# Kernel optimization log

Measured on AMD Instinct MI355X. Metric: run time of the kernel, lower is better.

## Reference

```python
import jax, jax.numpy as jnp
import numpy as np

N_EMBED = 384
T_MAX = 256
EPS = 1e-5


def layer_norm(x, gamma, beta):
    mu = jnp.mean(x, axis=-1, keepdims=True)
    var = jnp.mean(jnp.square(x - mu), axis=-1, keepdims=True)
    return (x - mu) * jax.lax.rsqrt(var + EPS) * gamma + beta


def setup_inputs() -> dict:
    key = jax.random.key(0)
    ks = jax.random.split(key, 12)
    B, T, C = 128, 256, N_EMBED
    s = lambda fan_in: 1.0 / np.sqrt(fan_in)
    return {
        "x": jax.random.normal(ks[0], (B, T, C), dtype=jnp.float32),
        "W_attn": jax.random.uniform(ks[1], (C, 3 * C), minval=-s(C), maxval=s(C), dtype=jnp.float32),
        "b_attn": jax.random.uniform(ks[2], (3 * C,), minval=-s(C), maxval=s(C), dtype=jnp.float32),
        "W_proj": jax.random.uniform(ks[3], (C, C), minval=-s(C), maxval=s(C), dtype=jnp.float32),
        "b_proj": jax.random.uniform(ks[4], (C,), minval=-s(C), maxval=s(C), dtype=jnp.float32),
        "ln1_g": jnp.ones((C,), jnp.float32),
        "ln1_b": jnp.zeros((C,), jnp.float32),
        "ln2_g": jnp.ones((C,), jnp.float32),
        "ln2_b": jnp.zeros((C,), jnp.float32),
        "W1": jax.random.uniform(ks[5], (C, 4 * C), minval=-s(C), maxval=s(C), dtype=jnp.float32),
        "b1": jax.random.uniform(ks[6], (4 * C,), minval=-s(C), maxval=s(C), dtype=jnp.float32),
        "W2": jax.random.uniform(ks[7], (4 * C, C), minval=-s(4 * C), maxval=s(4 * C), dtype=jnp.float32),
        "b2": jax.random.uniform(ks[8], (4 * C,)[:1] and (C,), minval=-s(4 * C), maxval=s(4 * C), dtype=jnp.float32),
    }


def reference(x, W_attn, b_attn, W_proj, b_proj, ln1_g, ln1_b, ln2_g, ln2_b, W1, b1, W2, b2):
    B, T, C = x.shape
    # --- pre-LN single-head causal self-attention ---
    h = layer_norm(x, ln1_g, ln1_b)
    qkv = h @ W_attn + b_attn                      # [B,T,3C]
    q, k, v = jnp.split(qkv, 3, axis=-1)           # each [B,T,C]
    att = jnp.einsum('btc,bsc->bts', q, k) * (1.0 / jnp.sqrt(jnp.float32(C)))
    causal = jnp.tril(jnp.ones((T, T), bool))
    att = jnp.where(causal, att, -jnp.inf)
    att = jax.nn.softmax(att, axis=-1)             # dropout is identity (eval)
    y = jnp.einsum('bts,bsc->btc', att, v)
    x = x + (y @ W_proj + b_proj)
    # --- pre-LN MLP ---
    h2 = layer_norm(x, ln2_g, ln2_b)
    x = x + (jax.nn.relu(h2 @ W1 + b1) @ W2 + b2)
    return x
```

## Files before the change

kernel.cpp:

```cpp
#include <hip/hip_runtime.h>
#include <hip/hip_bf16.h>

#define C_EMB 384
#define T_SEQ 256
#define B_BATCH 128
#define M_ROWS (B_BATCH * T_SEQ)
#define QKV_LD 1152
#define BK 64

typedef __bf16 bf16_8 __attribute__((ext_vector_type(8)));
typedef float f32x4 __attribute__((ext_vector_type(4)));

__device__ __forceinline__ void load16_lds(const __bf16* g, __bf16* l) {
    __builtin_amdgcn_global_load_lds(
        (const __attribute__((address_space(1))) unsigned int*)g,
        (__attribute__((address_space(3))) unsigned int*)l, 16, 0, 0);
}

__global__ __launch_bounds__(256) void cast_all_kernel(const float* __restrict__ Wa,
                                                       const float* __restrict__ Wp,
                                                       const float* __restrict__ W1,
                                                       const float* __restrict__ W2,
                                                       __bf16* __restrict__ Wa_t,
                                                       __bf16* __restrict__ Wp_t,
                                                       __bf16* __restrict__ W1_t,
                                                       __bf16* __restrict__ W2_t) {
    int bid = blockIdx.x;
    const float* W; __bf16* Wt; int K, N, tx_n;
    if (bid < 432)      { W = Wa; Wt = Wa_t; K = 384;  N = 1152; tx_n = 36; }
    else if (bid < 576) { bid -= 432; W = Wp; Wt = Wp_t; K = 384;  N = 384;  tx_n = 12; }
    else if (bid < 1152){ bid -= 576; W = W1; Wt = W1_t; K = 384;  N = 1536; tx_n = 48; }
    else                { bid -= 1152; W = W2; Wt = W2_t; K = 1536; N = 384;  tx_n = 12; }
    int n0 = (bid % tx_n) * 32, k0 = (bid / tx_n) * 32;

    __shared__ float t[32][33];
    int tx = threadIdx.x & 31, ty = threadIdx.x >> 5;
#pragma unroll
    for (int i = 0; i < 4; ++i)
        t[ty + i * 8][tx] = W[(size_t)(k0 + ty + i * 8) * N + n0 + tx];
    __syncthreads();
#pragma unroll
    for (int i = 0; i < 4; ++i) {
        int n = ty + i * 8;
        Wt[(size_t)(n0 + n) * K + k0 + tx] = (__bf16)t[tx][n];
    }
}

__global__ __launch_bounds__(384) void ln_kernel(const float* __restrict__ x,
                                                 const float* __restrict__ g,
                                                 const float* __restrict__ bta,
                                                 __bf16* __restrict__ out) {
    int row = blockIdx.x;
    int c = threadIdx.x;
    float v = x[(size_t)row * C_EMB + c];

    __shared__ float red[6];
    float s = v;
#pragma unroll
    for (int o = 32; o; o >>= 1) s += __shfl_down(s, o);
    if ((c & 63) == 0) red[c >> 6] = s;
    __syncthreads();
    float mu = (red[0] + red[1] + red[2] + red[3] + red[4] + red[5]) * (1.0f / C_EMB);

    float d = v - mu;
    float s2 = d * d;
#pragma unroll
    for (int o = 32; o; o >>= 1) s2 += __shfl_down(s2, o);
    __syncthreads();
    if ((c & 63) == 0) red[c >> 6] = s2;
    __syncthreads();
    float var = (red[0] + red[1] + red[2] + red[3] + red[4] + red[5]) * (1.0f / C_EMB);

    out[(size_t)row * C_EMB + c] = (__bf16)(d * rsqrtf(var + 1e-5f) * g[c] + bta[c]);
}

template <int K, int NFULL, bool RELU, bool ACCUM>
__global__ __launch_bounds__(512, 1) void gemm_pipe(const __bf16* __restrict__ A,
                                                    const __bf16* __restrict__ Bt,
                                                    const float* __restrict__ bias,
                                                    void* __restrict__ out_) {
    __shared__ __align__(16) __bf16 At[2][128 * 64];
    __shared__ __align__(16) __bf16 Bs[2][384 * 64];

    int tid = threadIdx.x;
    int wave = tid >> 6, lane = tid & 63;
    int wr = wave >> 1, wc = wave & 1;
    int quad = lane >> 4, l16 = lane & 15;
    int bm = blockIdx.y * 128;
    int n0 = blockIdx.x * 384;
    int srow = lane >> 3;
    int sunit = (lane & 7) ^ srow;

    const __bf16* asrc0 = A + (size_t)(bm + srow) * K + sunit * 8;
    const __bf16* bsrc0 = Bt + (size_t)(n0 + srow) * K + sunit * 8;

    auto stage = [&](int buf, int k0) {
#pragma unroll
        for (int t = 0; t < 2; ++t) {
            int g = t * 8 + wave;
            load16_lds(asrc0 + (size_t)(g * 8) * K + k0, &At[buf][g * 8 * 64]);
        }
#pragma unroll
        for (int t = 0; t < 6; ++t) {
            int g = t * 8 + wave;
            load16_lds(bsrc0 + (size_t)(g * 8) * K + k0, &Bs[buf][g * 8 * 64]);
        }
    };

    f32x4 acc[2][12] = {};

    stage(0, 0);
    asm volatile("s_waitcnt vmcnt(0)" ::: "memory");
    __builtin_amdgcn_sched_barrier(0);
    __builtin_amdgcn_s_barrier();

#pragma unroll 2
    for (int kt = 0; kt < K / BK; ++kt) {
        int cur = kt & 1;
        if (kt < K / BK - 1) stage(cur ^ 1, (kt + 1) * BK);

        bf16_8 af[2][2];
#pragma unroll
        for (int p = 0; p < 2; ++p)
#pragma unroll
            for (int i = 0; i < 2; ++i) {
                int row = wr * 32 + i * 16 + l16;
                int u = (p * 4 + quad) ^ (row & 7);
                af[i][p] = *reinterpret_cast<const bf16_8*>(&At[cur][row * 64 + u * 8]);
            }
#pragma unroll
        for (int p = 0; p < 2; ++p)
#pragma unroll
            for (int j = 0; j < 12; ++j) {
                int row = wc * 192 + j * 16 + l16;
                int u = (p * 4 + quad) ^ (row & 7);
                bf16_8 bf = *reinterpret_cast<const bf16_8*>(&Bs[cur][row * 64 + u * 8]);
                acc[0][j] = __builtin_amdgcn_mfma_f32_16x16x32_bf16(af[0][p], bf, acc[0][j], 0, 0, 0);
                acc[1][j] = __builtin_amdgcn_mfma_f32_16x16x32_bf16(af[1][p], bf, acc[1][j], 0, 0, 0);
            }

        asm volatile("s_waitcnt vmcnt(0)" ::: "memory");
        __builtin_amdgcn_sched_barrier(0);
        __builtin_amdgcn_s_barrier();
    }

#pragma unroll
    for (int i = 0; i < 2; ++i)
#pragma unroll
        for (int r = 0; r < 4; ++r) {
            int m = bm + wr * 32 + i * 16 + quad * 4 + r;
#pragma unroll
            for (int j = 0; j < 12; ++j) {
                int n = n0 + wc * 192 + j * 16 + l16;
                float v = acc[i][j][r] + bias[n];
                if (RELU) v = fmaxf(v, 0.0f);
                if (ACCUM) {
                    float* o = &((float*)out_)[(size_t)m * NFULL + n];
                    *o = *o + v;
                } else {
                    ((__bf16*)out_)[(size_t)m * NFULL + n] = (__bf16)v;
                }
            }
        }
}

template <int K, int NFULL, bool RELU, bool ACCUM>
__global__ __launch_bounds__(256, 2) void gemm_pipe2(const __bf16* __restrict__ A,
                                                     const __bf16* __restrict__ Bt,
                                                     const float* __restrict__ bias,
                                                     void* __restrict__ out_) {
    __shared__ __align__(16) __bf16 At[2][128 * 64];
    __shared__ __align__(16) __bf16 Bs[2][192 * 64];

    int tid = threadIdx.x;
    int wave = tid >> 6, lane = tid & 63;
    int quad = lane >> 4, l16 = lane & 15;
    int bm = blockIdx.y * 128;
    int n0 = blockIdx.x * 192;
    int srow = lane >> 3;
    int sunit = (lane & 7) ^ srow;

    const __bf16* asrc0 = A + (size_t)(bm + srow) * K + sunit * 8;
    const __bf16* bsrc0 = Bt + (size_t)(n0 + srow) * K + sunit * 8;

    auto stage = [&](int buf, int k0) {
#pragma unroll
        for (int t = 0; t < 4; ++t) {
            int g = t * 4 + wave;
            load16_lds(asrc0 + (size_t)(g * 8) * K + k0, &At[buf][g * 8 * 64]);
        }
#pragma unroll
        for (int t = 0; t < 6; ++t) {
            int g = t * 4 + wave;
            load16_lds(bsrc0 + (size_t)(g * 8) * K + k0, &Bs[buf][g * 8 * 64]);
        }
    };

    f32x4 acc[2][12] = {};

    stage(0, 0);
    asm volatile("s_waitcnt vmcnt(0)" ::: "memory");
    __builtin_amdgcn_sched_barrier(0);
    __builtin_amdgcn_s_barrier();

#pragma unroll 2
    for (int kt = 0; kt < K / BK; ++kt) {
        int cur = kt & 1;
        if (kt < K / BK - 1) stage(cur ^ 1, (kt + 1) * BK);

        bf16_8 af[2][2];
#pragma unroll
        for (int p = 0; p < 2; ++p)
#pragma unroll
            for (int i = 0; i < 2; ++i) {
                int row = wave * 32 + i * 16 + l16;
                int u = (p * 4 + quad) ^ (row & 7);
                af[i][p] = *reinterpret_cast<const bf16_8*>(&At[cur][row * 64 + u * 8]);
            }
#pragma unroll
        for (int p = 0; p < 2; ++p)
#pragma unroll
            for (int j = 0; j < 12; ++j) {
                int row = j * 16 + l16;
                int u = (p * 4 + quad) ^ (row & 7);
                bf16_8 bf = *reinterpret_cast<const bf16_8*>(&Bs[cur][row * 64 + u * 8]);
                acc[0][j] = __builtin_amdgcn_mfma_f32_16x16x32_bf16(af[0][p], bf, acc[0][j], 0, 0, 0);
                acc[1][j] = __builtin_amdgcn_mfma_f32_16x16x32_bf16(af[1][p], bf, acc[1][j], 0, 0, 0);
            }

        asm volatile("s_waitcnt vmcnt(0)" ::: "memory");
        __builtin_amdgcn_sched_barrier(0);
        __builtin_amdgcn_s_barrier();
    }

#pragma unroll
    for (int i = 0; i < 2; ++i)
#pragma unroll
        for (int r = 0; r < 4; ++r) {
            int m = bm + wave * 32 + i * 16 + quad * 4 + r;
#pragma unroll
            for (int j = 0; j < 12; ++j) {
                int n = n0 + j * 16 + l16;
                float v = acc[i][j][r] + bias[n];
                if (RELU) v = fmaxf(v, 0.0f);
                if (ACCUM) {
                    float* o = &((float*)out_)[(size_t)m * NFULL + n];
                    *o = *o + v;
                } else {
                    ((__bf16*)out_)[(size_t)m * NFULL + n] = (__bf16)v;
                }
            }
        }
}

__global__ __launch_bounds__(256) void proj_ln_kernel(const __bf16* __restrict__ A,
                                                      const __bf16* __restrict__ Bt,
                                                      const float* __restrict__ bias,
                                                      const float* __restrict__ resid,
                                                      const float* __restrict__ lng,
                                                      const float* __restrict__ lnb,
                                                      float* __restrict__ out,
                                                      __bf16* __restrict__ h) {
    __shared__ __align__(16) __bf16 As[2 * 64 * 32];
    __shared__ __align__(16) __bf16 Bs[2 * 384 * 32];
    __shared__ float red[2][2][64];

    int tid = threadIdx.x;
    int wave = tid >> 6, lane = tid & 63;
    int wr = wave >> 1, wc = wave & 1;
    int quad = lane >> 4, l16 = lane & 15;
    int bm = blockIdx.x * 64;
    int lrow = lane >> 2, lcol = (lane & 3) * 8;

    f32x4 acc[2][12] = {};

    for (int k0 = 0; k0 < C_EMB; k0 += BK) {
        const __bf16* Ab = A + (size_t)bm * C_EMB + k0;
        const __bf16* Bb = Bt + k0;
#pragma unroll
        for (int p = 0; p < 2; ++p) {
            {
                int r0 = wave * 16;
                load16_lds(Ab + (size_t)(r0 + lrow) * C_EMB + p * 32 + lcol,
                           &As[p * 64 * 32 + r0 * 32]);
            }
#pragma unroll
            for (int i = 0; i < 6; ++i) {
                int r0 = (i * 4 + wave) * 16;
                load16_lds(Bb + (size_t)(r0 + lrow) * C_EMB + p * 32 + lcol,
                           &Bs[p * 384 * 32 + r0 * 32]);
            }
        }
        __syncthreads();

        bf16_8 af[2][2], bf[12][2];
#pragma unroll
        for (int p = 0; p < 2; ++p) {
#pragma unroll
            for (int i = 0; i < 2; ++i)
                af[i][p] = *reinterpret_cast<const bf16_8*>(
                    &As[p * 64 * 32 + (wr * 32 + i * 16 + l16) * 32 + quad * 8]);
#pragma unroll
            for (int j = 0; j < 12; ++j)
                bf[j][p] = *reinterpret_cast<const bf16_8*>(
                    &Bs[p * 384 * 32 + (wc * 192 + j * 16 + l16) * 32 + quad * 8]);
        }
#pragma unroll
        for (int i = 0; i < 2; ++i)
#pragma unroll
            for (int j = 0; j < 12; ++j) {
                acc[i][j] = __builtin_amdgcn_mfma_f32_16x16x32_bf16(af[i][0], bf[j][0], acc[i][j], 0, 0, 0);
                acc[i][j] = __builtin_amdgcn_mfma_f32_16x16x32_bf16(af[i][1], bf[j][1], acc[i][j], 0, 0, 0);
            }
        __syncthreads();
    }

    float bia[12], gg[12], bb[12];
#pragma unroll
    for (int j = 0; j < 12; ++j) {
        int n = wc * 192 + j * 16 + l16;
        bia[j] = bias[n];
        gg[j] = lng[n];
        bb[j] = lnb[n];
    }

#pragma unroll
    for (int i = 0; i < 2; ++i)
#pragma unroll
        for (int r = 0; r < 4; ++r) {
            int rloc = wr * 32 + i * 16 + quad * 4 + r;
            int m = bm + rloc;
            float s = 0.0f, s2 = 0.0f;
#pragma unroll
            for (int j = 0; j < 12; ++j) {
                int n = wc * 192 + j * 16 + l16;
                float v = acc[i][j][r] + bia[j] + resid[(size_t)m * C_EMB + n];
                acc[i][j][r] = v;
                s += v;
                s2 += v * v;
            }
#pragma unroll
            for (int o = 8; o; o >>= 1) {
                s += __shfl_xor(s, o);
                s2 += __shfl_xor(s2, o);
            }
            if (l16 == 0) {
                red[0][wc][rloc] = s;
                red[1][wc][rloc] = s2;
            }
        }
    __syncthreads();

#pragma unroll
    for (int i = 0; i < 2; ++i)
#pragma unroll
        for (int r = 0; r < 4; ++r) {
            int rloc = wr * 32 + i * 16 + quad * 4 + r;
            int m = bm + rloc;
            float mu  = (red[0][0][rloc] + red[0][1][rloc]) * (1.0f / C_EMB);
            float ex2 = (red[1][0][rloc] + red[1][1][rloc]) * (1.0f / C_EMB);
            float rstd = rsqrtf(ex2 - mu * mu + 1e-5f);
#pragma unroll
            for (int j = 0; j < 12; ++j) {
                int n = wc * 192 + j * 16 + l16;
                float v = acc[i][j][r];
                out[(size_t)m * C_EMB + n] = v;
                h[(size_t)m * C_EMB + n] = (__bf16)((v - mu) * rstd * gg[j] + bb[j]);
            }
        }
}

__global__ __launch_bounds__(256) void vt_kernel(const __bf16* __restrict__ qkv,
                                                 __bf16* __restrict__ Vt) {
    __shared__ __align__(16) __bf16 t[32][72];
    int b = blockIdx.z, c0 = blockIdx.x * 64, s0 = blockIdx.y * 32;
    int tid = threadIdx.x;

    int tx = tid & 7, ty = tid >> 3;
    const __bf16* src = qkv + ((size_t)b * T_SEQ + s0 + ty) * QKV_LD + 768 + c0 + tx * 8;
    *reinterpret_cast<float4*>(&t[ty][tx * 8]) = *reinterpret_cast<const float4*>(src);
    __syncthreads();

    int sx = tid & 3, cy = tid >> 2;
    __align__(16) __bf16 tmp[8];
#pragma unroll
    for (int j = 0; j < 8; ++j) tmp[j] = t[sx * 8 + j][cy];
    *reinterpret_cast<float4*>(&Vt[((size_t)b * C_EMB + c0 + cy) * T_SEQ + s0 + sx * 8]) =
        *reinterpret_cast<float4*>(tmp);
}

__global__ __launch_bounds__(256) void qks_mfma(const __bf16* __restrict__ qkv,
                                                __bf16* __restrict__ P) {
    int b = blockIdx.y;
    int bx = blockIdx.x;
    int bm = bx * 128;
    int ntiles = bx + 1;
    const __bf16* Ab0 = qkv + (size_t)b * T_SEQ * QKV_LD;
    const __bf16* Bb0 = Ab0 + 384;

    __shared__ __align__(16) __bf16 As[2 * 128 * 32];
    __shared__ __align__(16) __bf16 Bs[2 * 128 * 32];
    __shared__ float red[2][2][128];

    int tid = threadIdx.x;
    int wave = tid >> 6, lane = tid & 63;
    int wr = wave >> 1, wc = wave & 1;
    int quad = lane >> 4, l16 = lane & 15;
    int lrow = lane >> 2, lcol = (lane & 3) * 8;

    f32x4 acc[2][4][4] = {};

#pragma unroll
    for (int nt = 0; nt < 2; ++nt) {
        if (nt < ntiles) {
            int bn = nt * 128;
            for (int k0 = 0; k0 < C_EMB; k0 += BK) {
                const __bf16* Ab = Ab0 + (size_t)bm * QKV_LD + k0;
                const __bf16* Bb = Bb0 + (size_t)bn * QKV_LD + k0;
#pragma unroll
                for (int p = 0; p < 2; ++p)
#pragma unroll
                    for (int i = 0; i < 2; ++i) {
                        int r0 = (i * 4 + wave) * 16;
                        load16_lds(Ab + (size_t)(r0 + lrow) * QKV_LD + p * 32 + lcol,
                                   &As[p * 128 * 32 + r0 * 32]);
                        load16_lds(Bb + (size_t)(r0 + lrow) * QKV_LD + p * 32 + lcol,
                                   &Bs[p * 128 * 32 + r0 * 32]);
                    }
                __syncthreads();

                bf16_8 af[4][2], bf[4][2];
#pragma unroll
                for (int p = 0; p < 2; ++p)
#pragma unroll
                    for (int i = 0; i < 4; ++i) {
                        af[i][p] = *reinterpret_cast<const bf16_8*>(
                            &As[p * 128 * 32 + (wr * 64 + i * 16 + l16) * 32 + quad * 8]);
                        bf[i][p] = *reinterpret_cast<const bf16_8*>(
                            &Bs[p * 128 * 32 + (wc * 64 + i * 16 + l16) * 32 + quad * 8]);
                    }
#pragma unroll
                for (int i = 0; i < 4; ++i)
#pragma unroll
                    for (int j = 0; j < 4; ++j) {
                        acc[nt][i][j] = __builtin_amdgcn_mfma_f32_16x16x32_bf16(af[i][0], bf[j][0], acc[nt][i][j], 0, 0, 0);
                        acc[nt][i][j] = __builtin_amdgcn_mfma_f32_16x16x32_bf16(af[i][1], bf[j][1], acc[nt][i][j], 0, 0, 0);
                    }
                __syncthreads();
            }
        }
    }

    const float scale = 0.05103103630798288f;

#pragma unroll
    for (int i = 0; i < 4; ++i)
#pragma unroll
        for (int r = 0; r < 4; ++r) {
            int rloc = wr * 64 + i * 16 + quad * 4 + r;
            int t = bm + rloc;
            float m = -INFINITY;
#pragma unroll
            for (int nt = 0; nt < 2; ++nt)
#pragma unroll
                for (int j = 0; j < 4; ++j) {
                    int n = nt * 128 + wc * 64 + j * 16 + l16;
                    bool ok = (nt < ntiles) && (n <= t);
                    float v = acc[nt][i][j][r] * scale;
                    m = fmaxf(m, ok ? v : -INFINITY);
                }
#pragma unroll
            for (int o = 8; o; o >>= 1) m = fmaxf(m, __shfl_xor(m, o));
            if (l16 == 0) red[0][wc][rloc] = m;
        }
    __syncthreads();

#pragma unroll
    for (int i = 0; i < 4; ++i)
#pragma unroll
        for (int r = 0; r < 4; ++r) {
            int rloc = wr * 64 + i * 16 + quad * 4 + r;
            int t = bm + rloc;
            float M = fmaxf(red[0][0][rloc], red[0][1][rloc]);
            float s = 0.0f;
#pragma unroll
            for (int nt = 0; nt < 2; ++nt)
#pragma unroll
                for (int j = 0; j < 4; ++j) {
                    int n = nt * 128 + wc * 64 + j * 16 + l16;
                    bool ok = (nt < ntiles) && (n <= t);
                    float p = ok ? __expf(acc[nt][i][j][r] * scale - M) : 0.0f;
                    acc[nt][i][j][r] = p;
                    s += p;
                }
#pragma unroll
            for (int o = 8; o; o >>= 1) s += __shfl_xor(s, o);
            if (l16 == 0) red[1][wc][rloc] = s;
        }
    __syncthreads();

    __bf16* Pb_ = P + (size_t)b * T_SEQ * T_SEQ;
#pragma unroll
    for (int i = 0; i < 4; ++i)
#pragma unroll
        for (int r = 0; r < 4; ++r) {
            int rloc = wr * 64 + i * 16 + quad * 4 + r;
            float inv = 1.0f / (red[1][0][rloc] + red[1][1][rloc]);
#pragma unroll
            for (int nt = 0; nt < 2; ++nt)
                if (nt < ntiles)
#pragma unroll
                    for (int j = 0; j < 4; ++j) {
                        int n = nt * 128 + wc * 64 + j * 16 + l16;
                        Pb_[(size_t)(bm + rloc) * T_SEQ + n] = (__bf16)(acc[nt][i][j][r] * inv);
                    }
        }
}

__global__ __launch_bounds__(256) void pv_mfma(const __bf16* __restrict__ P,
                                               const __bf16* __restrict__ Vt,
                                               __bf16* __restrict__ y) {
    int b = blockIdx.z;
    int bm = blockIdx.y * 128, bn = blockIdx.x * 128;
    const __bf16* Ab0 = P + (size_t)b * T_SEQ * T_SEQ;
    const __bf16* Bb0 = Vt + (size_t)b * C_EMB * T_SEQ;

    __shared__ __align__(16) __bf16 As[2 * 128 * 32];
    __shared__ __align__(16) __bf16 Bs[2 * 128 * 32];

    int tid = threadIdx.x;
    int wave = tid >> 6, lane = tid & 63;
    int wr = wave >> 1, wc = wave & 1;
    int quad = lane >> 4, l16 = lane & 15;
    int lrow = lane >> 2, lcol = (lane & 3) * 8;

    f32x4 acc[4][4] = {};

    int kmax = bm + 128;
    for (int k0 = 0; k0 < kmax; k0 += BK) {
        const __bf16* Ab = Ab0 + (size_t)bm * T_SEQ + k0;
        const __bf16* Bb = Bb0 + (size_t)bn * T_SEQ + k0;
#pragma unroll
        for (int p = 0; p < 2; ++p)
#pragma unroll
            for (int i = 0; i < 2; ++i) {
                int r0 = (i * 4 + wave) * 16;
                load16_lds(Ab + (size_t)(r0 + lrow) * T_SEQ + p * 32 + lcol,
                           &As[p * 128 * 32 + r0 * 32]);
                load16_lds(Bb + (size_t)(r0 + lrow) * T_SEQ + p * 32 + lcol,
                           &Bs[p * 128 * 32 + r0 * 32]);
            }
        __syncthreads();

        bf16_8 af[4][2], bf[4][2];
#pragma unroll
        for (int p = 0; p < 2; ++p)
#pragma unroll
            for (int i = 0; i < 4; ++i) {
                af[i][p] = *reinterpret_cast<const bf16_8*>(
                    &As[p * 128 * 32 + (wr * 64 + i * 16 + l16) * 32 + quad * 8]);
                bf[i][p] = *reinterpret_cast<const bf16_8*>(
                    &Bs[p * 128 * 32 + (wc * 64 + i * 16 + l16) * 32 + quad * 8]);
            }
#pragma unroll
        for (int i = 0; i < 4; ++i)
#pragma unroll
            for (int j = 0; j < 4; ++j) {
                acc[i][j] = __builtin_amdgcn_mfma_f32_16x16x32_bf16(af[i][0], bf[j][0], acc[i][j], 0, 0, 0);
                acc[i][j] = __builtin_amdgcn_mfma_f32_16x16x32_bf16(af[i][1], bf[j][1], acc[i][j], 0, 0, 0);
            }
        __syncthreads();
    }

#pragma unroll
    for (int i = 0; i < 4; ++i) {
#pragma unroll
        for (int r = 0; r < 4; ++r) {
            int m = bm + wr * 64 + i * 16 + quad * 4 + r;
#pragma unroll
            for (int j = 0; j < 4; ++j) {
                int n = bn + wc * 64 + j * 16 + l16;
                y[((size_t)b * T_SEQ + m) * C_EMB + n] = (__bf16)acc[i][j][r];
            }
        }
    }
}

extern "C" void kernel_launch(void* const* d_in, const int* in_sizes, int n_in,
                              void* d_out, int out_size, void* d_ws, size_t ws_size,
                              hipStream_t stream) {
    const float* x      = (const float*)d_in[0];
    const float* W_attn = (const float*)d_in[1];
    const float* b_attn = (const float*)d_in[2];
    const float* W_proj = (const float*)d_in[3];
    const float* b_proj = (const float*)d_in[4];
    const float* ln1_g  = (const float*)d_in[5];
    const float* ln1_b  = (const float*)d_in[6];
    const float* ln2_g  = (const float*)d_in[7];
    const float* ln2_b  = (const float*)d_in[8];
    const float* W1     = (const float*)d_in[9];
    const float* b1     = (const float*)d_in[10];
    const float* W2     = (const float*)d_in[11];
    const float* b2     = (const float*)d_in[12];
    float* out = (float*)d_out;

    __bf16* Wattn_t = (__bf16*)d_ws;
    __bf16* Wproj_t = Wattn_t + (size_t)1152 * 384;
    __bf16* W1_t    = Wproj_t + (size_t)384 * 384;
    __bf16* W2_t    = W1_t + (size_t)1536 * 384;
    __bf16* h       = W2_t + (size_t)384 * 1536;
    __bf16* yb      = h + (size_t)M_ROWS * 384;
    __bf16* qkv     = yb + (size_t)M_ROWS * 384;
    float*  S       = (float*)(qkv + (size_t)M_ROWS * QKV_LD);
    __bf16* Pb      = (__bf16*)(S + (size_t)B_BATCH * T_SEQ * T_SEQ);
    __bf16* Vt      = Pb + (size_t)B_BATCH * T_SEQ * T_SEQ;
    __bf16* ff      = qkv;

    cast_all_kernel<<<1728, 256, 0, stream>>>(W_attn, W_proj, W1, W2,
                                              Wattn_t, Wproj_t, W1_t, W2_t);

    ln_kernel<<<M_ROWS, 384, 0, stream>>>(x, ln1_g, ln1_b, h);
    gemm_pipe<384, 1152, false, false><<<dim3(1152 / 384, M_ROWS / 128), 512, 0, stream>>>(
        h, Wattn_t, b_attn, qkv);
    vt_kernel<<<dim3(C_EMB / 64, T_SEQ / 32, B_BATCH), 256, 0, stream>>>(qkv, Vt);
    qks_mfma<<<dim3(2, B_BATCH), 256, 0, stream>>>(qkv, Pb);
    pv_mfma<<<dim3(C_EMB / 128, T_SEQ / 128, B_BATCH), 256, 0, stream>>>(Pb, Vt, yb);
    proj_ln_kernel<<<M_ROWS / 64, 256, 0, stream>>>(yb, Wproj_t, b_proj, x,
                                                    ln2_g, ln2_b, out, h);
    gemm_pipe2<384, 1536, true, false><<<dim3(1536 / 192, M_ROWS / 128), 256, 0, stream>>>(
        h, W1_t, b1, ff);
    gemm_pipe2<1536, 384, false, true><<<dim3(384 / 192, M_ROWS / 128), 256, 0, stream>>>(
        ff, W2_t, b2, out);
}
```

Measured before the change: 437.1 us.

## Triple-buffer MLP GEMMs with 8-wave blocks and swizzled tile order

Replaces the double-buffered 4-wave MLP GEMM with a 512-thread, 8-wave version that splits each 128x192 tile into a 2x... grid of per-wave subtiles. It uses three LDS stages with a partial vmcnt wait, so loads for step k+2 overlap compute on step k, and only one barrier is issued per iteration. Block indices are remapped in groups of 8 to improve L2 reuse of A and B tiles. LDS use grows to 120 KB and occupancy drops to one block per CU.

Result: slower. 450.7 us (+3.1%).

```diff
diff --git a/kernel.cpp b/kernel.cpp
--- a/kernel.cpp
+++ b/kernel.cpp
@@ -164,19 +164,26 @@
         }
 }
 
-template <int K, int NFULL, bool RELU, bool ACCUM>
-__global__ __launch_bounds__(256, 2) void gemm_pipe2(const __bf16* __restrict__ A,
+template <int K, int NFULL, int GX, bool RELU, bool ACCUM>
+__global__ __launch_bounds__(512, 1) void gemm_pipe3(const __bf16* __restrict__ A,
                                                      const __bf16* __restrict__ Bt,
                                                      const float* __restrict__ bias,
                                                      void* __restrict__ out_) {
-    __shared__ __align__(16) __bf16 At[2][128 * 64];
-    __shared__ __align__(16) __bf16 Bs[2][192 * 64];
+    constexpr int NT = K / BK;
+    __shared__ __align__(16) __bf16 At[3][128 * 64];
+    __shared__ __align__(16) __bf16 Bs[3][192 * 64];
 
     int tid = threadIdx.x;
     int wave = tid >> 6, lane = tid & 63;
+    int wr = wave >> 1, wc = wave & 1;
     int quad = lane >> 4, l16 = lane & 15;
-    int bm = blockIdx.y * 128;
-    int n0 = blockIdx.x * 192;
+
+    constexpr int NWG = GX * (M_ROWS / 128);
+    int lin = blockIdx.x + blockIdx.y * GX;
+    int swz = (lin & 7) * (NWG / 8) + (lin >> 3);
+    int bm = (swz / GX) * 128;
+    int n0 = (swz % GX) * 192;
+
     int srow = lane >> 3;
     int sunit = (lane & 7) ^ srow;
 
@@ -185,62 +192,68 @@
 
     auto stage = [&](int buf, int k0) {
 #pragma unroll
-        for (int t = 0; t < 4; ++t) {
-            int g = t * 4 + wave;
+        for (int t = 0; t < 2; ++t) {
+            int g = t * 8 + wave;
             load16_lds(asrc0 + (size_t)(g * 8) * K + k0, &At[buf][g * 8 * 64]);
         }
 #pragma unroll
-        for (int t = 0; t < 6; ++t) {
-            int g = t * 4 + wave;
+        for (int t = 0; t < 3; ++t) {
+            int g = t * 8 + wave;
             load16_lds(bsrc0 + (size_t)(g * 8) * K + k0, &Bs[buf][g * 8 * 64]);
         }
     };
 
-    f32x4 acc[2][12] = {};
+    f32x4 acc[2][6] = {};
+
+    auto compute = [&](int cb) {
+        bf16_8 af[2][2];
+#pragma unroll
+        for (int p = 0; p < 2; ++p)
+#pragma unroll
+            for (int i = 0; i < 2; ++i) {
+                int row = wr * 32 + i * 16 + l16;
+                int u = (p * 4 + quad) ^ (row & 7);
+                af[i][p] = *reinterpret_cast<const bf16_8*>(&At[cb][row * 64 + u * 8]);
+            }
+#pragma unroll
+        for (int p = 0; p < 2; ++p)
+#pragma unroll
+            for (int j = 0; j < 6; ++j) {
+                int row = wc * 96 + j * 16 + l16;
+                int u = (p * 4 + quad) ^ (row & 7);
+                bf16_8 bf = *reinterpret_cast<const bf16_8*>(&Bs[cb][row * 64 + u * 8]);
+                acc[0][j] = __builtin_amdgcn_mfma_f32_16x16x32_bf16(af[0][p], bf, acc[0][j], 0, 0, 0);
+                acc[1][j] = __builtin_amdgcn_mfma_f32_16x16x32_bf16(af[1][p], bf, acc[1][j], 0, 0, 0);
+            }
+    };
 
     stage(0, 0);
+    stage(1, BK);
+
+    for (int kt = 0; kt < NT - 2; ++kt) {
+        asm volatile("s_waitcnt vmcnt(5)" ::: "memory");
+        __builtin_amdgcn_sched_barrier(0);
+        __builtin_amdgcn_s_barrier();
+        stage((kt + 2) % 3, (kt + 2) * BK);
+        compute(kt % 3);
+    }
+    asm volatile("s_waitcnt vmcnt(5)" ::: "memory");
+    __builtin_amdgcn_sched_barrier(0);
+    __builtin_amdgcn_s_barrier();
+    compute((NT - 2) % 3);
     asm volatile("s_waitcnt vmcnt(0)" ::: "memory");
     __builtin_amdgcn_sched_barrier(0);
     __builtin_amdgcn_s_barrier();
-
-#pragma unroll 2
-    for (int kt = 0; kt < K / BK; ++kt) {
-        int cur = kt & 1;
-        if (kt < K / BK - 1) stage(cur ^ 1, (kt + 1) * BK);
-
-        bf16_8 af[2][2];
-#pragma unroll
-        for (int p = 0; p < 2; ++p)
-#pragma unroll
-            for (int i = 0; i < 2; ++i) {
-                int row = wave * 32 + i * 16 + l16;
-                int u = (p * 4 + quad) ^ (row & 7);
-                af[i][p] = *reinterpret_cast<const bf16_8*>(&At[cur][row * 64 + u * 8]);
-            }
-#pragma unroll
-        for (int p = 0; p < 2; ++p)
-#pragma unroll
-            for (int j = 0; j < 12; ++j) {
-                int row = j * 16 + l16;
-                int u = (p * 4 + quad) ^ (row & 7);
-                bf16_8 bf = *reinterpret_cast<const bf16_8*>(&Bs[cur][row * 64 + u * 8]);
-                acc[0][j] = __builtin_amdgcn_mfma_f32_16x16x32_bf16(af[0][p], bf, acc[0][j], 0, 0, 0);
-                acc[1][j] = __builtin_amdgcn_mfma_f32_16x16x32_bf16(af[1][p], bf, acc[1][j], 0, 0, 0);
-            }
-
-        asm volatile("s_waitcnt vmcnt(0)" ::: "memory");
-        __builtin_amdgcn_sched_barrier(0);
-        __builtin_amdgcn_s_barrier();
-    }
+    compute((NT - 1) % 3);
 
 #pragma unroll
     for (int i = 0; i < 2; ++i)
 #pragma unroll
         for (int r = 0; r < 4; ++r) {
-            int m = bm + wave * 32 + i * 16 + quad * 4 + r;
-#pragma unroll
-            for (int j = 0; j < 12; ++j) {
-                int n = n0 + j * 16 + l16;
+            int m = bm + wr * 32 + i * 16 + quad * 4 + r;
+#pragma unroll
+            for (int j = 0; j < 6; ++j) {
+                int n = n0 + wc * 96 + j * 16 + l16;
                 float v = acc[i][j][r] + bias[n];
                 if (RELU) v = fmaxf(v, 0.0f);
                 if (ACCUM) {
@@ -627,8 +640,8 @@
     pv_mfma<<<dim3(C_EMB / 128, T_SEQ / 128, B_BATCH), 256, 0, stream>>>(Pb, Vt, yb);
     proj_ln_kernel<<<M_ROWS / 64, 256, 0, stream>>>(yb, Wproj_t, b_proj, x,
                                                     ln2_g, ln2_b, out, h);
-    gemm_pipe2<384, 1536, true, false><<<dim3(1536 / 192, M_ROWS / 128), 256, 0, stream>>>(
+    gemm_pipe3<384, 1536, 8, true, false><<<dim3(1536 / 192, M_ROWS / 128), 512, 0, stream>>>(
         h, W1_t, b1, ff);
-    gemm_pipe2<1536, 384, false, true><<<dim3(384 / 192, M_ROWS / 128), 256, 0, stream>>>(
+    gemm_pipe3<1536, 384, 2, false, true><<<dim3(384 / 192, M_ROWS / 128), 512, 0, stream>>>(
         ff, W2_t, b2, out);
 }
```
